# Performance work log

Hardware: AMD Instinct MI355X
Metric: run time of the kernel (lower is better)

The kernel has to match this reference:

```python
import jax, jax.numpy as jnp
import numpy as np

B, S, HIDDEN = 2, 2048, 2048
HQ, HKV, D = 16, 4, 128
EPS = 1e-6
SCALE = D ** -0.5


def _deinterleave(x):
    # [..., D] interleaved pairs -> [x0,x2,...,x1,x3,...] (half layout)
    *lead, d = x.shape
    return x.reshape(*lead, d // 2, 2).swapaxes(-1, -2).reshape(*lead, d)


def _interleave(x):
    # inverse of _deinterleave
    *lead, d = x.shape
    return x.reshape(*lead, 2, d // 2).swapaxes(-1, -2).reshape(*lead, d)


def _rotate_half(x):
    x1, x2 = jnp.split(x, 2, axis=-1)
    return jnp.concatenate([-x2, x1], axis=-1)


def _rmsnorm(x, w):
    var = jnp.mean(jnp.square(x), axis=-1, keepdims=True)
    return x * jax.lax.rsqrt(var + EPS) * w


def setup_inputs() -> dict:
    key = jax.random.key(0)
    k0, k1, k2, k3, k4 = jax.random.split(key, 5)
    hidden_states = jax.random.normal(k0, (B, S, HIDDEN), jnp.float32)
    cos = jax.random.uniform(k1, (S, D), jnp.float32, -1.0, 1.0)
    sin = jax.random.uniform(k2, (S, D), jnp.float32, -1.0, 1.0)
    qkv_w = jax.random.normal(k3, ((HQ + 2 * HKV) * D, HIDDEN), jnp.float32) * 0.02
    qk_norm_w = jnp.ones((D,), jnp.float32)
    o_w = jax.random.normal(k4, (HIDDEN, HQ * D), jnp.float32) * 0.02
    return {"hidden_states": hidden_states, "cos": cos, "sin": sin,
            "qkv_w": qkv_w, "qk_norm_w": qk_norm_w, "o_w": o_w}


def reference(hidden_states, cos, sin, qkv_w, qk_norm_w, o_w):
    b, s, _ = hidden_states.shape
    qkv = jnp.einsum('bsh,oh->bso', hidden_states, qkv_w)  # [B,S,(HQ+2HKV)*D]
    q = qkv[..., : HQ * D].reshape(b, s, HQ, D)
    k = qkv[..., HQ * D:(HQ + HKV) * D].reshape(b, s, HKV, D)
    v = qkv[..., (HQ + HKV) * D:].reshape(b, s, HKV, D)

    # interleaved-layout RoPE: deinterleave -> rotate-half RoPE -> re-interleave
    q, k = _deinterleave(q), _deinterleave(k)
    cs = cos[None, :, None, :]
    sn = sin[None, :, None, :]
    q = q * cs + _rotate_half(q) * sn
    k = k * cs + _rotate_half(k) * sn
    q, k = _interleave(q), _interleave(k)

    # QK RMSNorm (shared weight over head_dim)
    q = _rmsnorm(q, qk_norm_w)
    k = _rmsnorm(k, qk_norm_w)

    # causal GQA attention
    g = HQ // HKV
    qg = q.reshape(b, s, HKV, g, D)
    scores = jnp.einsum('bshgd,bthd->bhgst', qg, k) * SCALE  # [B,HKV,g,S,S]
    causal = jnp.tril(jnp.ones((s, s), bool))
    scores = jnp.where(causal, scores, jnp.finfo(scores.dtype).min)
    probs = jax.nn.softmax(scores, axis=-1)
    attn = jnp.einsum('bhgst,bthd->bshgd', probs, v).reshape(b, s, HQ * D)

    return jnp.einsum('bsd,od->bso', attn, o_w)
```

## Files before the change

kernel.cpp:

```cpp
#include <hip/hip_runtime.h>
#include <hip/hip_bf16.h>

typedef __bf16 bf16_t;
typedef bf16_t bf16x8 __attribute__((ext_vector_type(8)));
typedef float f32x4 __attribute__((ext_vector_type(4)));
typedef float f32x16 __attribute__((ext_vector_type(16)));
typedef unsigned short u16;
typedef unsigned int u32;

#define B_    2
#define S_    2048
#define HID   2048
#define NQKV  3072
#define HQ_   16
#define HKV_  4
#define D_    128
#define QSCALE_ 0.12751879526600565f

__device__ __forceinline__ u16 f2b(float f) {
    __hip_bfloat16 h = __float2bfloat16(f);
    return *reinterpret_cast<u16*>(&h);
}
__device__ __forceinline__ float b2f(u32 u) {
    u32 v = u << 16;
    float f;
    __builtin_memcpy(&f, &v, 4);
    return f;
}

__global__ __launch_bounds__(256) void cvt_f32_bf16(const float* __restrict__ in,
                                                    u16* __restrict__ out, int n4) {
    int i = blockIdx.x * 256 + threadIdx.x;
    if (i >= n4) return;
    float4 v = reinterpret_cast<const float4*>(in)[i];
    ushort4 o;
    o.x = f2b(v.x); o.y = f2b(v.y); o.z = f2b(v.z); o.w = f2b(v.w);
    reinterpret_cast<ushort4*>(out)[i] = o;
}

template<bool BF16OUT>
__global__ __launch_bounds__(512, 1) void gemm128x256(const u16* __restrict__ A,
                                                      const u16* __restrict__ Bm,
                                                      void* __restrict__ Cv,
                                                      int M, int N, int K) {
    extern __shared__ __align__(16) char smem[];

    const int tid  = threadIdx.x;
    const int lane = tid & 63;
    const int wid  = tid >> 6;
    const int wr = wid >> 2, wc = wid & 3;
    const int lrow = lane & 15, lgrp = lane >> 4;
    const int swz  = (lrow & 7) << 4;

    const int gx = gridDim.x;
    const int nwg = gx * gridDim.y;
    const int id = blockIdx.x + blockIdx.y * gx;
    const int swid = (id & 7) * (nwg >> 3) + (id >> 3);
    const int m0 = (swid % gx) * 128, n0 = (swid / gx) * 256;

    const int stRow = tid >> 3;
    const int stCol = ((((tid & 7) * 16) ^ ((stRow & 7) << 4)) >> 1);
    const u16* aBase = A  + (size_t)(m0 + stRow) * K + stCol;
    const u16* bBase = Bm + (size_t)(n0 + stRow) * K + stCol;

    auto glds = [&](const u16* g, u16* l) {
        __builtin_amdgcn_global_load_lds(
            (const __attribute__((address_space(1))) void*)g,
            (__attribute__((address_space(3))) void*)l, 16, 0, 0);
    };
    auto stA = [&](int buf, int k0) {
        u16* d = (u16*)(smem + buf * 49152) + tid * 8;
        glds(aBase + k0, d);
        glds(aBase + (size_t)64 * K + k0, d + 512 * 8);
    };
    auto stB = [&](int buf, int h, int k0) {
        u16* d = (u16*)(smem + buf * 49152 + 16384 + h * 16384) + tid * 8;
        const u16* g = bBase + (size_t)(128 * h) * K + k0;
        glds(g, d);
        glds(g + (size_t)64 * K, d + 512 * 8);
    };

    f32x4 acc[4][4] = {};
    const int KT = K >> 6;

    stA(0, 0); stB(0, 0, 0); stB(0, 1, 0);
    asm volatile("s_waitcnt vmcnt(0)" ::: "memory");
    __builtin_amdgcn_s_barrier();

    for (int t = 0; t < KT; ++t) {
        const int cur = t & 1;
        const int kn  = (t + 1) << 6;
        const bool pf = (t + 1 < KT);
        const char* aT = smem + cur * 49152;
        const char* bT = aT + 16384;

        auto ldA = [&](int mi, int ks) -> bf16x8 {
            int row = wr * 64 + mi * 16 + lrow;
            return *(const bf16x8*)(aT + row * 128 + ((ks * 64 + lgrp * 16) ^ swz));
        };
        auto ldB = [&](int ni, int ks) -> bf16x8 {
            int row = wc * 64 + ni * 16 + lrow;
            return *(const bf16x8*)(bT + row * 128 + ((ks * 64 + lgrp * 16) ^ swz));
        };

        bf16x8 a[4][2], b[2][2], b2[2][2];

        #pragma unroll
        for (int mi = 0; mi < 4; ++mi) { a[mi][0] = ldA(mi, 0); a[mi][1] = ldA(mi, 1); }
        #pragma unroll
        for (int ni = 0; ni < 2; ++ni) { b[ni][0] = ldB(ni, 0); b[ni][1] = ldB(ni, 1); }
        if (pf) { stA(cur ^ 1, kn); stB(cur ^ 1, 0, kn); stB(cur ^ 1, 1, kn); }
        __builtin_amdgcn_s_barrier();
        __builtin_amdgcn_s_setprio(1);
        #pragma unroll
        for (int mi = 0; mi < 4; ++mi)
            #pragma unroll
            for (int ni = 0; ni < 2; ++ni) {
                acc[mi][ni] = __builtin_amdgcn_mfma_f32_16x16x32_bf16(a[mi][0], b[ni][0], acc[mi][ni], 0, 0, 0);
                acc[mi][ni] = __builtin_amdgcn_mfma_f32_16x16x32_bf16(a[mi][1], b[ni][1], acc[mi][ni], 0, 0, 0);
            }
        __builtin_amdgcn_s_setprio(0);

        #pragma unroll
        for (int ni = 0; ni < 2; ++ni) { b2[ni][0] = ldB(ni + 2, 0); b2[ni][1] = ldB(ni + 2, 1); }
        __builtin_amdgcn_s_barrier();
        __builtin_amdgcn_s_setprio(1);
        #pragma unroll
        for (int mi = 0; mi < 4; ++mi)
            #pragma unroll
            for (int ni = 0; ni < 2; ++ni) {
                acc[mi][ni + 2] = __builtin_amdgcn_mfma_f32_16x16x32_bf16(a[mi][0], b2[ni][0], acc[mi][ni + 2], 0, 0, 0);
                acc[mi][ni + 2] = __builtin_amdgcn_mfma_f32_16x16x32_bf16(a[mi][1], b2[ni][1], acc[mi][ni + 2], 0, 0, 0);
            }
        __builtin_amdgcn_s_setprio(0);
        if (pf) {
            asm volatile("s_waitcnt vmcnt(0)" ::: "memory");
            __builtin_amdgcn_s_barrier();
        }
    }

    #pragma unroll
    for (int mi = 0; mi < 4; ++mi)
        #pragma unroll
        for (int ni = 0; ni < 4; ++ni) {
            int r = m0 + wr * 64 + mi * 16 + lgrp * 4;
            int c = n0 + wc * 64 + ni * 16 + lrow;
            if (BF16OUT) {
                u16* o = (u16*)Cv + (size_t)r * N + c;
                #pragma unroll
                for (int i = 0; i < 4; ++i) o[(size_t)i * N] = f2b(acc[mi][ni][i]);
            } else {
                float* p = (float*)Cv + (size_t)r * N + c;
                #pragma unroll
                for (int i = 0; i < 4; ++i) p[(size_t)i * N] = acc[mi][ni][i];
            }
        }
}

__global__ __launch_bounds__(256) void rope_norm_split(const u16* __restrict__ qkvb,
                                                       const float* __restrict__ cosb,
                                                       const float* __restrict__ sinb,
                                                       const float* __restrict__ nw,
                                                       u16* __restrict__ qb,
                                                       u16* __restrict__ kb,
                                                       u16* __restrict__ vb) {
    const int row  = blockIdx.x;
    const int b    = row >> 11;
    const int s    = row & 2047;
    const int wave = threadIdx.x >> 6;
    const int lane = threadIdx.x & 63;
    const u16* base = qkvb + (size_t)row * NQKV;

    const float c0 = cosb[s * 128 + lane];
    const float c1 = cosb[s * 128 + 64 + lane];
    const float s0 = sinb[s * 128 + lane];
    const float s1 = sinb[s * 128 + 64 + lane];
    const float w0 = nw[2 * lane];
    const float w1 = nw[2 * lane + 1];

    for (int h = wave; h < HQ_ + HKV_; h += 4) {
        u32 xw = *(const u32*)(base + h * 128 + 2 * lane);
        float x0 = b2f(xw & 0xffffu), x1 = b2f(xw >> 16);
        float y0 = x0 * c0 - x1 * s0;
        float y1 = x1 * c1 + x0 * s1;
        float ss = y0 * y0 + y1 * y1;
        #pragma unroll
        for (int off = 32; off; off >>= 1) ss += __shfl_xor(ss, off);
        float r = rsqrtf(ss * (1.0f / 128.0f) + 1e-6f);
        float o0 = y0 * r * w0, o1 = y1 * r * w1;
        if (h < HQ_) {
            u32 pack = (u32)f2b(o0 * QSCALE_) | ((u32)f2b(o1 * QSCALE_) << 16);
            *(u32*)(qb + ((size_t)(b * HQ_ + h) * S_ + s) * D_ + 2 * lane) = pack;
        } else {
            u32 pack = (u32)f2b(o0) | ((u32)f2b(o1) << 16);
            *(u32*)(kb + ((size_t)(b * HKV_ + (h - HQ_)) * S_ + s) * D_ + 2 * lane) = pack;
        }
    }
    {
        int h = wave;
        u32 xw = *(const u32*)(base + (HQ_ + HKV_) * 128 + h * 128 + 2 * lane);
        *(u32*)(vb + ((size_t)(b * HKV_ + h) * S_ + s) * D_ + 2 * lane) = xw;
    }
}

__global__ __launch_bounds__(256) void transpose_v(const u16* __restrict__ vb,
                                                   u16* __restrict__ vtb) {
    __shared__ u16 t[64][72];
    const int s0 = blockIdx.x * 64, d0 = blockIdx.y * 64, bh = blockIdx.z;
    const u16* src = vb  + (size_t)bh * S_ * D_;
    u16*       dst = vtb + (size_t)bh * D_ * S_;
    const int tid = threadIdx.x;

    {
        int r = tid >> 3, c8 = (tid & 7) * 8;
        #pragma unroll
        for (int p = 0; p < 2; p++) {
            int rr = r + p * 32;
            *(uint4*)&t[rr][c8] = *(const uint4*)(src + (size_t)(s0 + rr) * D_ + d0 + c8);
        }
    }
    __syncthreads();
    {
        int dd = tid & 63;
        int sb = (tid >> 6) * 8;
        #pragma unroll
        for (int p = 0; p < 2; p++) {
            int ss8 = sb + p * 32;
            union { u16 u[8]; uint4 v; } pk;
            #pragma unroll
            for (int j = 0; j < 8; j++) pk.u[j] = t[ss8 + j][dd];
            *(uint4*)(dst + (size_t)(d0 + dd) * S_ + s0 + ss8) = pk.v;
        }
    }
}

__global__ __launch_bounds__(256, 2) void attn_fwd3(const u16* __restrict__ qb,
                                                    const u16* __restrict__ kb,
                                                    const u16* __restrict__ vtb,
                                                    u16* __restrict__ attn) {
    __shared__ __align__(16) u16 Ks[2][64 * 128];
    __shared__ __align__(16) u16 Vs[2][128 * 64];

    const int bh  = blockIdx.y;
    const int qt  = (bh < 16) ? (15 - (int)blockIdx.x) : (int)blockIdx.x;
    const int b   = bh >> 4, hq = bh & 15, hkv = hq >> 2;
    const int tid = threadIdx.x;
    const int wave = tid >> 6, lane = tid & 63;
    const int l31 = lane & 31, hi = lane >> 5;
    const int swz = (l31 & 7) << 4;

    const u16* Q  = qb  + (size_t)(b * HQ_  + hq ) * S_ * D_;
    const u16* Kp = kb  + (size_t)(b * HKV_ + hkv) * S_ * D_;
    const u16* Vt = vtb + (size_t)(b * HKV_ + hkv) * D_ * S_;
    const int q0w = qt * 128 + wave * 32;
    const int qg  = q0w + l31;

    int kSrc[4], vSrc[4], cLds[4];
    #pragma unroll
    for (int p = 0; p < 4; p++) {
        int c = tid + p * 256;
        int kr = c >> 4, kc = ((c & 15) * 16) ^ ((kr & 7) << 4);
        kSrc[p] = kr * D_ + (kc >> 1);
        int vr = c >> 3, vc = ((c & 7) * 16) ^ ((vr & 7) << 4);
        vSrc[p] = vr * S_ + (vc >> 1);
        cLds[p] = c * 16;
    }

    auto STAGE = [&](int buf, int kv0s) {
        const u16* kbase = Kp + (size_t)kv0s * D_;
        const u16* vbase = Vt + kv0s;
        #pragma unroll
        for (int p = 0; p < 4; p++)
            __builtin_amdgcn_global_load_lds(
                (const __attribute__((address_space(1))) void*)(kbase + kSrc[p]),
                (__attribute__((address_space(3))) void*)((char*)Ks[buf] + cLds[p]), 16, 0, 0);
        #pragma unroll
        for (int p = 0; p < 4; p++)
            __builtin_amdgcn_global_load_lds(
                (const __attribute__((address_space(1))) void*)(vbase + vSrc[p]),
                (__attribute__((address_space(3))) void*)((char*)Vs[buf] + cLds[p]), 16, 0, 0);
    };

    bf16x8 qf[8];
    #pragma unroll
    for (int ds = 0; ds < 8; ds++)
        qf[ds] = *(const bf16x8*)(Q + (size_t)qg * D_ + ds * 16 + hi * 8);

    float m_run = -1e30f, l_run = 0.f;
    f32x16 oacc[4] = {};

    const int nkt = 2 * qt + 2;
    STAGE(0, 0);

    for (int kt = 0; kt < nkt; kt++) {
        const int cur = kt & 1;
        const int kv0 = kt * 64;
        if (kt + 1 < nkt) {
            STAGE(cur ^ 1, kv0 + 64);
            asm volatile("s_waitcnt vmcnt(8)" ::: "memory");
        } else {
            asm volatile("s_waitcnt vmcnt(0)" ::: "memory");
        }
        __builtin_amdgcn_s_barrier();

        const char* ksb = (const char*)Ks[cur];
        const char* vsb = (const char*)Vs[cur];
        const char* rb0 = ksb + l31 * 256;
        const char* rb1 = rb0 + 32 * 256;
        bf16x8 kA[8], kB[8];
        #pragma unroll
        for (int ds = 0; ds < 8; ds++) kA[ds] = *(const bf16x8*)(rb0 + ((ds * 32 + hi * 16) ^ swz));
        #pragma unroll
        for (int ds = 0; ds < 8; ds++) kB[ds] = *(const bf16x8*)(rb1 + ((ds * 32 + hi * 16) ^ swz));

        f32x16 sc[2] = {};
        __builtin_amdgcn_s_setprio(1);
        #pragma unroll
        for (int ds = 0; ds < 8; ds++)
            sc[0] = __builtin_amdgcn_mfma_f32_32x32x16_bf16(kA[ds], qf[ds], sc[0], 0, 0, 0);
        #pragma unroll
        for (int ds = 0; ds < 8; ds++)
            sc[1] = __builtin_amdgcn_mfma_f32_32x32x16_bf16(kB[ds], qf[ds], sc[1], 0, 0, 0);
        __builtin_amdgcn_s_setprio(0);

        bf16x8 vf[4][4];
        #pragma unroll
        for (int ks = 0; ks < 4; ks++)
            #pragma unroll
            for (int d4 = 0; d4 < 4; d4++)
                vf[ks][d4] = *(const bf16x8*)(vsb + (d4 * 32 + l31) * 128
                                                  + ((ks * 32 + hi * 16) ^ swz));
        __builtin_amdgcn_s_barrier();

        if (kv0 + 63 > q0w) {
            #pragma unroll
            for (int blk = 0; blk < 2; blk++)
                #pragma unroll
                for (int r = 0; r < 16; r++) {
                    int kvg = kv0 + blk * 32 + (r & 3) + 8 * (r >> 2) + 4 * hi;
                    if (kvg > qg) sc[blk][r] = -1e30f;
                }
        }

        float t16[16];
        #pragma unroll
        for (int r = 0; r < 16; r++) t16[r] = fmaxf(sc[0][r], sc[1][r]);
        #pragma unroll
        for (int r = 0; r < 8; r++) t16[r] = fmaxf(t16[r], t16[r + 8]);
        #pragma unroll
        for (int r = 0; r < 4; r++) t16[r] = fmaxf(t16[r], t16[r + 4]);
        float mt = fmaxf(fmaxf(t16[0], t16[1]), fmaxf(t16[2], t16[3]));
        mt = fmaxf(mt, __shfl_xor(mt, 32));

        bool noDefer = !__all(mt <= m_run + 8.0f);
        float mnew = m_run;
        if (noDefer) {
            mnew = fmaxf(m_run, mt);
            float alpha = __builtin_amdgcn_exp2f(m_run - mnew);
            l_run *= alpha;
            #pragma unroll
            for (int d4 = 0; d4 < 4; d4++)
                #pragma unroll
                for (int r = 0; r < 16; r++) oacc[d4][r] *= alpha;
            m_run = mnew;
        }

        float la = 0.f;
        u32 pk0[8], pk1[8];
        #pragma unroll
        for (int g = 0; g < 4; g++)
            #pragma unroll
            for (int e = 0; e < 2; e++) {
                float a0 = __builtin_amdgcn_exp2f(sc[0][g * 4 + 2 * e]     - mnew);
                float b0 = __builtin_amdgcn_exp2f(sc[0][g * 4 + 2 * e + 1] - mnew);
                float a1 = __builtin_amdgcn_exp2f(sc[1][g * 4 + 2 * e]     - mnew);
                float b1 = __builtin_amdgcn_exp2f(sc[1][g * 4 + 2 * e + 1] - mnew);
                la += (a0 + b0) + (a1 + b1);
                pk0[g * 2 + e] = (u32)f2b(a0) | ((u32)f2b(b0) << 16);
                pk1[g * 2 + e] = (u32)f2b(a1) | ((u32)f2b(b1) << 16);
            }
        la += __shfl_xor(la, 32);
        l_run += la;

        u32 qk0[8], qk1[8];
        #pragma unroll
        for (int i = 0; i < 8; i++) {
            qk0[i] = __shfl_xor(pk0[i], 32);
            qk1[i] = __shfl_xor(pk1[i], 32);
        }

        #pragma unroll
        for (int ks = 0; ks < 4; ks++) {
            const int i0 = (ks & 1) * 4;
            union { u32 w[4]; bf16x8 v; } pfv;
            if (ks & 2) {
                pfv.w[0] = hi ? qk1[i0 + 2] : pk1[i0 + 0];
                pfv.w[1] = hi ? qk1[i0 + 3] : pk1[i0 + 1];
                pfv.w[2] = hi ? pk1[i0 + 2] : qk1[i0 + 0];
                pfv.w[3] = hi ? pk1[i0 + 3] : qk1[i0 + 1];
            } else {
                pfv.w[0] = hi ? qk0[i0 + 2] : pk0[i0 + 0];
                pfv.w[1] = hi ? qk0[i0 + 3] : pk0[i0 + 1];
                pfv.w[2] = hi ? pk0[i0 + 2] : qk0[i0 + 0];
                pfv.w[3] = hi ? pk0[i0 + 3] : qk0[i0 + 1];
            }
            __builtin_amdgcn_s_setprio(1);
            #pragma unroll
            for (int d4 = 0; d4 < 4; d4++)
                oacc[d4] = __builtin_amdgcn_mfma_f32_32x32x16_bf16(vf[ks][d4], pfv.v, oacc[d4], 0, 0, 0);
            __builtin_amdgcn_s_setprio(0);
        }
    }

    const float inv = 1.0f / l_run;
    u16* sl = (u16*)Ks + wave * (32 * 128);
    #pragma unroll
    for (int d4 = 0; d4 < 4; d4++)
        #pragma unroll
        for (int rp = 0; rp < 8; rp++) {
            int dbyte = d4 * 64 + 16 * (rp >> 1) + 8 * hi + 4 * (rp & 1);
            u32 w = (u32)f2b(oacc[d4][rp * 2] * inv)
                  | ((u32)f2b(oacc[d4][rp * 2 + 1] * inv) << 16);
            *(u32*)((char*)sl + l31 * 256 + (dbyte ^ swz)) = w;
        }
    #pragma unroll
    for (int j = 0; j < 8; j++) {
        int c = lane + j * 64;
        int qL = c >> 4, dc = c & 15;
        uint4 v = *(uint4*)((char*)sl + qL * 256 + ((dc * 16) ^ ((qL & 7) << 4)));
        int qrow = qt * 128 + wave * 32 + qL;
        *(uint4*)(attn + (size_t)(b * S_ + qrow) * (HQ_ * D_) + hq * D_ + dc * 8) = v;
    }
}

extern "C" void kernel_launch(void* const* d_in, const int* in_sizes, int n_in,
                              void* d_out, int out_size, void* d_ws, size_t ws_size,
                              hipStream_t stream) {
    const float* hidden = (const float*)d_in[0];
    const float* cosb   = (const float*)d_in[1];
    const float* sinb   = (const float*)d_in[2];
    const float* qkvw   = (const float*)d_in[3];
    const float* nw     = (const float*)d_in[4];
    const float* ow     = (const float*)d_in[5];
    float* out = (float*)d_out;

    const size_t M  = (size_t)B_ * S_;
    char* ws = (char*)d_ws;
    size_t off = 0;
    u16*   hb    = (u16*)(ws + off); off += M * HID * 2;
    u16*   wqkvb = (u16*)(ws + off); off += (size_t)NQKV * HID * 2;
    u16*   wob   = (u16*)(ws + off); off += (size_t)HID * (HQ_ * D_) * 2;
    u16*   qkvb  = (u16*)(ws + off); off += M * NQKV * 2;
    u16*   qb2   = (u16*)(ws + off); off += (size_t)B_ * HQ_  * S_ * D_ * 2;
    u16*   kb2   = (u16*)(ws + off); off += (size_t)B_ * HKV_ * S_ * D_ * 2;
    u16*   vb2   = (u16*)(ws + off); off += (size_t)B_ * HKV_ * S_ * D_ * 2;
    u16*   vtb   = (u16*)(ws + off); off += (size_t)B_ * HKV_ * S_ * D_ * 2;
    u16*   attn  = hb;

    {
        int n4 = (int)(M * HID / 4);
        cvt_f32_bf16<<<(n4 + 255) / 256, 256, 0, stream>>>(hidden, hb, n4);
    }
    {
        int n4 = NQKV * HID / 4;
        cvt_f32_bf16<<<(n4 + 255) / 256, 256, 0, stream>>>(qkvw, wqkvb, n4);
    }
    {
        int n4 = HID * (HQ_ * D_) / 4;
        cvt_f32_bf16<<<(n4 + 255) / 256, 256, 0, stream>>>(ow, wob, n4);
    }

    const int smemSz = 98304;
    auto* g1 = gemm128x256<true>;
    auto* g2 = gemm128x256<false>;
    hipFuncSetAttribute(reinterpret_cast<const void*>(g1),
                        hipFuncAttributeMaxDynamicSharedMemorySize, smemSz);
    hipFuncSetAttribute(reinterpret_cast<const void*>(g2),
                        hipFuncAttributeMaxDynamicSharedMemorySize, smemSz);

    gemm128x256<true><<<dim3(M / 128, NQKV / 256), 512, smemSz, stream>>>(
        hb, wqkvb, qkvb, (int)M, NQKV, HID);

    rope_norm_split<<<(int)M, 256, 0, stream>>>(qkvb, cosb, sinb, nw, qb2, kb2, vb2);

    transpose_v<<<dim3(S_ / 64, D_ / 64, B_ * HKV_), 256, 0, stream>>>(vb2, vtb);

    attn_fwd3<<<dim3(16, B_ * HQ_), 256, 0, stream>>>(qb2, kb2, vtb, attn);

    gemm128x256<false><<<dim3(M / 128, HID / 256), 512, smemSz, stream>>>(
        attn, wob, out, (int)M, HID, HQ_ * D_);
}
```

Baseline: 221.2 us.

## Merge conversion launches, restructure GEMM prefetch sync, split attention MFMA chains

Fuses the three fp32-to-bf16 conversion kernels into a single launch to cut launch overhead. Reorders the GEMM main loop so the next tile's global-to-LDS loads are issued at the top of each iteration, followed by a partial vmcnt wait and one barrier, instead of waiting for all loads at the end. This drops the barrier between the two MFMA halves. Splits the QK^T MFMA accumulation in attention into four independent chains to shorten dependency stalls, at the cost of extra accumulator registers and a final add. The GEMM change relies on the vmcnt(6) count matching the number of loads issued per stage; if that count is wrong, stale LDS data could be read.

New measurement: 219.1 us. No clear change (-1.0%).

```diff
diff --git a/kernel.cpp b/kernel.cpp
--- a/kernel.cpp
+++ b/kernel.cpp
@@ -28,14 +28,19 @@
     return f;
 }
 
-__global__ __launch_bounds__(256) void cvt_f32_bf16(const float* __restrict__ in,
-                                                    u16* __restrict__ out, int n4) {
+__global__ __launch_bounds__(256) void cvt3_f32_bf16(const float* __restrict__ i0, u16* __restrict__ o0, int n0,
+                                                     const float* __restrict__ i1, u16* __restrict__ o1, int n1,
+                                                     const float* __restrict__ i2, u16* __restrict__ o2, int n2) {
     int i = blockIdx.x * 256 + threadIdx.x;
-    if (i >= n4) return;
-    float4 v = reinterpret_cast<const float4*>(in)[i];
+    const float* src; u16* dst; int idx;
+    if (i < n0)           { src = i0; dst = o0; idx = i; }
+    else if (i < n0 + n1) { src = i1; dst = o1; idx = i - n0; }
+    else if (i < n0 + n1 + n2) { src = i2; dst = o2; idx = i - n0 - n1; }
+    else return;
+    float4 v = reinterpret_cast<const float4*>(src)[idx];
     ushort4 o;
     o.x = f2b(v.x); o.y = f2b(v.y); o.z = f2b(v.z); o.w = f2b(v.w);
-    reinterpret_cast<ushort4*>(out)[i] = o;
+    reinterpret_cast<ushort4*>(dst)[idx] = o;
 }
 
 template<bool BF16OUT>
@@ -84,8 +89,6 @@
     const int KT = K >> 6;
 
     stA(0, 0); stB(0, 0, 0); stB(0, 1, 0);
-    asm volatile("s_waitcnt vmcnt(0)" ::: "memory");
-    __builtin_amdgcn_s_barrier();
 
     for (int t = 0; t < KT; ++t) {
         const int cur = t & 1;
@@ -93,6 +96,14 @@
         const bool pf = (t + 1 < KT);
         const char* aT = smem + cur * 49152;
         const char* bT = aT + 16384;
+
+        if (pf) {
+            stA(cur ^ 1, kn); stB(cur ^ 1, 0, kn); stB(cur ^ 1, 1, kn);
+            asm volatile("s_waitcnt vmcnt(6)" ::: "memory");
+        } else {
+            asm volatile("s_waitcnt vmcnt(0)" ::: "memory");
+        }
+        __builtin_amdgcn_s_barrier();
 
         auto ldA = [&](int mi, int ks) -> bf16x8 {
             int row = wr * 64 + mi * 16 + lrow;
@@ -109,8 +120,6 @@
         for (int mi = 0; mi < 4; ++mi) { a[mi][0] = ldA(mi, 0); a[mi][1] = ldA(mi, 1); }
         #pragma unroll
         for (int ni = 0; ni < 2; ++ni) { b[ni][0] = ldB(ni, 0); b[ni][1] = ldB(ni, 1); }
-        if (pf) { stA(cur ^ 1, kn); stB(cur ^ 1, 0, kn); stB(cur ^ 1, 1, kn); }
-        __builtin_amdgcn_s_barrier();
         __builtin_amdgcn_s_setprio(1);
         #pragma unroll
         for (int mi = 0; mi < 4; ++mi)
@@ -123,7 +132,6 @@
 
         #pragma unroll
         for (int ni = 0; ni < 2; ++ni) { b2[ni][0] = ldB(ni + 2, 0); b2[ni][1] = ldB(ni + 2, 1); }
-        __builtin_amdgcn_s_barrier();
         __builtin_amdgcn_s_setprio(1);
         #pragma unroll
         for (int mi = 0; mi < 4; ++mi)
@@ -133,10 +141,7 @@
                 acc[mi][ni + 2] = __builtin_amdgcn_mfma_f32_16x16x32_bf16(a[mi][1], b2[ni][1], acc[mi][ni + 2], 0, 0, 0);
             }
         __builtin_amdgcn_s_setprio(0);
-        if (pf) {
-            asm volatile("s_waitcnt vmcnt(0)" ::: "memory");
-            __builtin_amdgcn_s_barrier();
-        }
+        __builtin_amdgcn_s_barrier();
     }
 
     #pragma unroll
@@ -313,15 +318,19 @@
         #pragma unroll
         for (int ds = 0; ds < 8; ds++) kB[ds] = *(const bf16x8*)(rb1 + ((ds * 32 + hi * 16) ^ swz));
 
-        f32x16 sc[2] = {};
+        f32x16 s0a = {}, s0b = {}, s1a = {}, s1b = {};
         __builtin_amdgcn_s_setprio(1);
         #pragma unroll
-        for (int ds = 0; ds < 8; ds++)
-            sc[0] = __builtin_amdgcn_mfma_f32_32x32x16_bf16(kA[ds], qf[ds], sc[0], 0, 0, 0);
-        #pragma unroll
-        for (int ds = 0; ds < 8; ds++)
-            sc[1] = __builtin_amdgcn_mfma_f32_32x32x16_bf16(kB[ds], qf[ds], sc[1], 0, 0, 0);
+        for (int ds = 0; ds < 4; ds++) {
+            s0a = __builtin_amdgcn_mfma_f32_32x32x16_bf16(kA[ds],     qf[ds],     s0a, 0, 0, 0);
+            s0b = __builtin_amdgcn_mfma_f32_32x32x16_bf16(kA[ds + 4], qf[ds + 4], s0b, 0, 0, 0);
+            s1a = __builtin_amdgcn_mfma_f32_32x32x16_bf16(kB[ds],     qf[ds],     s1a, 0, 0, 0);
+            s1b = __builtin_amdgcn_mfma_f32_32x32x16_bf16(kB[ds + 4], qf[ds + 4], s1b, 0, 0, 0);
+        }
         __builtin_amdgcn_s_setprio(0);
+        f32x16 sc[2];
+        sc[0] = s0a + s0b;
+        sc[1] = s1a + s1b;
 
         bf16x8 vf[4][4];
         #pragma unroll
@@ -458,16 +467,13 @@
     u16*   attn  = hb;
 
     {
-        int n4 = (int)(M * HID / 4);
-        cvt_f32_bf16<<<(n4 + 255) / 256, 256, 0, stream>>>(hidden, hb, n4);
-    }
-    {
-        int n4 = NQKV * HID / 4;
-        cvt_f32_bf16<<<(n4 + 255) / 256, 256, 0, stream>>>(qkvw, wqkvb, n4);
-    }
-    {
-        int n4 = HID * (HQ_ * D_) / 4;
-        cvt_f32_bf16<<<(n4 + 255) / 256, 256, 0, stream>>>(ow, wob, n4);
+        int n0 = (int)(M * HID / 4);
+        int n1 = NQKV * HID / 4;
+        int n2 = HID * (HQ_ * D_) / 4;
+        int nt = n0 + n1 + n2;
+        cvt3_f32_bf16<<<(nt + 255) / 256, 256, 0, stream>>>(hidden, hb, n0,
+                                                            qkvw, wqkvb, n1,
+                                                            ow, wob, n2);
     }
 
     const int smemSz = 98304;
```
